# Optimization experiments

Hardware: AMD Instinct MI355X
Metric: run time of the kernel (lower is better)

## Reference

```python
import jax, jax.numpy as jnp
import numpy as np

B, N, E, H = 4, 2048, 1024, 16
D = E // H
SCALE = 1.0 / np.sqrt(D).astype(np.float32)


def setup_inputs() -> dict:
    key = jax.random.key(0)
    ks = jax.random.split(key, 8)
    xq = jax.random.normal(ks[0], (B, N, E), jnp.float32)
    xk = jax.random.normal(ks[1], (B, N, E), jnp.float32)
    xv = jax.random.normal(ks[2], (B, N, E), jnp.float32)
    # causal mask: True means 'masked out' (matches masked_fill_ semantics)
    attn_mask = jnp.triu(jnp.ones((N, N), dtype=bool), k=1)[None, None]
    Wq = jax.random.normal(ks[3], (E, E), jnp.float32) / np.sqrt(E)
    Wk = jax.random.normal(ks[4], (E, E), jnp.float32) / np.sqrt(E)
    Wv = jax.random.normal(ks[5], (E, E), jnp.float32) / np.sqrt(E)
    Wo = jax.random.normal(ks[6], (E, E), jnp.float32) / np.sqrt(E)
    bo = jnp.zeros((E,), jnp.float32)
    return {"xq": xq, "xk": xk, "xv": xv, "attn_mask": attn_mask,
            "Wq": Wq, "Wk": Wk, "Wv": Wv, "Wo": Wo, "bo": bo}


def _split_heads(x):
    # [B, N, E] -> [B, H, N, D]
    return x.reshape(B, N, H, D).transpose(0, 2, 1, 3)


def reference(xq, xk, xv, attn_mask, Wq, Wk, Wv, Wo, bo):
    # torch nn.Linear: y = x @ W.T
    q = _split_heads(xq @ Wq.T)
    k = _split_heads(xk @ Wk.T)
    v = _split_heads(xv @ Wv.T)
    scores = SCALE * jnp.einsum('bhqd,bhkd->bhqk', q, k)
    scores = jnp.where(attn_mask, -jnp.inf, scores)
    attn = jax.nn.softmax(scores, axis=-1)
    out = jnp.einsum('bhqk,bhkd->bhqd', attn, v)
    out = out.transpose(0, 2, 1, 3).reshape(B, N, E)  # merge heads
    return out @ Wo.T + bo
```

## Files before the change

### kernel.cpp

```cpp
#include <hip/hip_runtime.h>
#include <hip/hip_bf16.h>
#include <stdint.h>
#include <stddef.h>

#define B_ 4
#define N_ 2048
#define E_ 1024
#define H_ 16
#define D_ 64

using bf16 = __hip_bfloat16;
typedef __bf16 bf16x8 __attribute__((ext_vector_type(8)));
typedef float  f32x4  __attribute__((ext_vector_type(4)));

__device__ inline bf16x8 load8(const float* p) {
    f32x4 a = *(const f32x4*)p;
    f32x4 b = *(const f32x4*)(p + 4);
    bf16x8 r;
#pragma unroll
    for (int e = 0; e < 4; e++) { r[e] = (__bf16)a[e]; r[e + 4] = (__bf16)b[e]; }
    return r;
}
__device__ inline void store_elem(float* C, size_t idx, float v) { C[idx] = v; }
__device__ inline void store_elem(bf16* C, size_t idx, float v) {
    C[idx] = __float2bfloat16(v);
}

__device__ inline void async_stage16(const bf16* g, bf16* l) {
    __builtin_amdgcn_global_load_lds(
        (const __attribute__((address_space(1))) uint32_t*)g,
        (__attribute__((address_space(3))) uint32_t*)l, 16, 0, 0);
}
__device__ inline void manual_stage16(const float* g, bf16* l) {
    *(bf16x8*)l = load8(g);
}

__global__ __launch_bounds__(256) void cvt_all(
    const float* __restrict__ w0, const float* __restrict__ w1,
    const float* __restrict__ w2, const float* __restrict__ w3,
    bf16* __restrict__ wd,
    const float* __restrict__ x0, const float* __restrict__ x1,
    const float* __restrict__ x2,
    bf16* __restrict__ xd0, bf16* __restrict__ xd1, bf16* __restrict__ xd2)
{
    int bx = blockIdx.x;
    const float* s; bf16* d;
    if (bx < 2048) {
        const int seg = bx >> 9;
        s = seg == 0 ? w0 : seg == 1 ? w1 : seg == 2 ? w2 : w3;
        d = wd + (size_t)seg * (E_ * E_);
        bx &= 511;
    } else {
        bx -= 2048;
        const int seg = bx >> 12;
        s = seg == 0 ? x0 : seg == 1 ? x1 : x2;
        d = seg == 0 ? xd0 : seg == 1 ? xd1 : xd2;
        bx &= 4095;
    }
    const size_t off = ((size_t)bx * 256 + threadIdx.x) * 8;
    *(bf16x8*)&d[off] = load8(s + off);
}

struct GemmB { const void* A[3]; void* C[3]; };

template <typename TA, typename TC>
__global__ __launch_bounds__(256) void gemm_bt(
    GemmB batch, const bf16* __restrict__ Wb, const float* __restrict__ bias)
{
    __shared__ bf16 As[128 * 32];
    __shared__ bf16 Bs[128 * 32];

    const TA*   __restrict__ A = (const TA*)batch.A[blockIdx.z];
    TC*         __restrict__ C = (TC*)batch.C[blockIdx.z];
    const bf16* __restrict__ W = Wb + (size_t)blockIdx.z * (E_ * E_);

    const int tid  = threadIdx.x;
    const int lane = tid & 63;
    const int wave = tid >> 6;
    const int wr   = wave >> 1;
    const int wc   = wave & 1;
    const int r    = lane & 15;
    const int quad = lane >> 4;

    const int m0 = blockIdx.y * 128;
    const int n0 = blockIdx.x * 128;

    const int row0 = tid >> 2,         cc0 = (tid & 3) * 8;
    const int row1 = (tid + 256) >> 2, cc1 = cc0;

    f32x4 acc[4][4];
#pragma unroll
    for (int i = 0; i < 4; i++)
#pragma unroll
        for (int j = 0; j < 4; j++)
            acc[i][j] = {0.0f, 0.0f, 0.0f, 0.0f};

    for (int k0 = 0; k0 < E_; k0 += 32) {
        __syncthreads();
        if constexpr (__is_same(TA, bf16)) {
            async_stage16(&A[(size_t)(m0 + row0) * E_ + k0 + cc0], &As[tid * 8]);
            async_stage16(&A[(size_t)(m0 + row1) * E_ + k0 + cc1], &As[(tid + 256) * 8]);
        } else {
            manual_stage16(&A[(size_t)(m0 + row0) * E_ + k0 + cc0], &As[tid * 8]);
            manual_stage16(&A[(size_t)(m0 + row1) * E_ + k0 + cc1], &As[(tid + 256) * 8]);
        }
        async_stage16(&W[(size_t)(n0 + row0) * E_ + k0 + cc0], &Bs[tid * 8]);
        async_stage16(&W[(size_t)(n0 + row1) * E_ + k0 + cc1], &Bs[(tid + 256) * 8]);
        __syncthreads();

        bf16x8 a[4], b[4];
#pragma unroll
        for (int mt = 0; mt < 4; mt++)
            a[mt] = *(const bf16x8*)&As[(wr * 64 + mt * 16 + r) * 32 + quad * 8];
#pragma unroll
        for (int nt = 0; nt < 4; nt++)
            b[nt] = *(const bf16x8*)&Bs[(wc * 64 + nt * 16 + r) * 32 + quad * 8];
#pragma unroll
        for (int mt = 0; mt < 4; mt++)
#pragma unroll
            for (int nt = 0; nt < 4; nt++)
                acc[mt][nt] = __builtin_amdgcn_mfma_f32_16x16x32_bf16(
                    a[mt], b[nt], acc[mt][nt], 0, 0, 0);
    }

#pragma unroll
    for (int mt = 0; mt < 4; mt++) {
#pragma unroll
        for (int nt = 0; nt < 4; nt++) {
            const int col = n0 + wc * 64 + nt * 16 + r;
            float bv = bias ? bias[col] : 0.0f;
#pragma unroll
            for (int rg = 0; rg < 4; rg++) {
                const int row = m0 + wr * 64 + mt * 16 + quad * 4 + rg;
                store_elem(C, (size_t)row * E_ + col, acc[mt][nt][rg] + bv);
            }
        }
    }
}

__global__ __launch_bounds__(256) void attn_fwd(
    const bf16* __restrict__ q, const bf16* __restrict__ k,
    const bf16* __restrict__ v, bf16* __restrict__ o)
{
    constexpr int LS = 72;
    __shared__ bf16 Ks[64 * LS];
    __shared__ bf16 Vt[64 * LS];
    __shared__ bf16 Ps[128 * LS];

    const int tid  = threadIdx.x;
    const int lane = tid & 63;
    const int wave = tid >> 6;
    const int r    = lane & 15;
    const int quad = lane >> 4;

    const int bh = blockIdx.y;
    const int b  = bh >> 4;
    const int h  = bh & 15;
    const int xb = gridDim.x - 1 - blockIdx.x;
    const int q0 = xb * 128;

    const size_t basek = (size_t)b * N_ * E_ + (size_t)h * D_;

    bf16x8 qB[2][2];
#pragma unroll
    for (int s = 0; s < 2; s++) {
        const size_t qrow =
            ((size_t)b * N_ + q0 + wave * 32 + s * 16 + r) * E_ + h * D_;
        qB[s][0] = *(const bf16x8*)&q[qrow + quad * 8];
        qB[s][1] = *(const bf16x8*)&q[qrow + quad * 8 + 32];
    }

    float m_i[2] = {-1e30f, -1e30f};
    float l_i[2] = {0.0f, 0.0f};
    f32x4 o_acc[4][2];
#pragma unroll
    for (int dt = 0; dt < 4; dt++)
#pragma unroll
        for (int s = 0; s < 2; s++)
            o_acc[dt][s] = {0.0f, 0.0f, 0.0f, 0.0f};

    const int ntiles = 2 * xb + 2;

    const int key0 = tid >> 3;
    const int key1 = key0 + 32;
    const int ck   = (tid & 7) * 8;
    const int kp   = tid & 31;
    const int cv   = (tid >> 5) * 8;

    bf16x8 kpre0 = *(const bf16x8*)&k[basek + (size_t)key0 * E_ + ck];
    bf16x8 kpre1 = *(const bf16x8*)&k[basek + (size_t)key1 * E_ + ck];
    bf16x8 vp0   = *(const bf16x8*)&v[basek + (size_t)(2 * kp) * E_ + cv];
    bf16x8 vp1   = *(const bf16x8*)&v[basek + (size_t)(2 * kp + 1) * E_ + cv];

    for (int t = 0; t < ntiles; t++) {
        __syncthreads();
        *(bf16x8*)&Ks[key0 * LS + ck] = kpre0;
        *(bf16x8*)&Ks[key1 * LS + ck] = kpre1;
#pragma unroll
        for (int e = 0; e < 8; e++) {
            union { __bf16 hh[2]; uint32_t u; } pk;
            pk.hh[0] = vp0[e]; pk.hh[1] = vp1[e];
            *(uint32_t*)&Vt[(cv + e) * LS + 2 * kp] = pk.u;
        }
        __syncthreads();

        if (t + 1 < ntiles) {
            const size_t j1 = (size_t)(t + 1) * 64;
            kpre0 = *(const bf16x8*)&k[basek + (j1 + key0) * E_ + ck];
            kpre1 = *(const bf16x8*)&k[basek + (j1 + key1) * E_ + ck];
            vp0   = *(const bf16x8*)&v[basek + (j1 + 2 * kp) * E_ + cv];
            vp1   = *(const bf16x8*)&v[basek + (j1 + 2 * kp + 1) * E_ + cv];
        }

        f32x4 sf[4][2];
#pragma unroll
        for (int mt = 0; mt < 4; mt++)
#pragma unroll
            for (int s = 0; s < 2; s++)
                sf[mt][s] = {0.0f, 0.0f, 0.0f, 0.0f};
#pragma unroll
        for (int ks = 0; ks < 2; ks++)
#pragma unroll
            for (int mt = 0; mt < 4; mt++) {
                bf16x8 ka = *(const bf16x8*)&Ks[(mt * 16 + r) * LS + ks * 32 + quad * 8];
#pragma unroll
                for (int s = 0; s < 2; s++)
                    sf[mt][s] = __builtin_amdgcn_mfma_f32_16x16x32_bf16(
                        ka, qB[s][ks], sf[mt][s], 0, 0, 0);
            }

        if (t >= ntiles - 2) {
#pragma unroll
            for (int mt = 0; mt < 4; mt++)
#pragma unroll
                for (int s = 0; s < 2; s++) {
                    const int qgl = q0 + wave * 32 + s * 16 + r;
#pragma unroll
                    for (int rg = 0; rg < 4; rg++) {
                        const int kgl = t * 64 + mt * 16 + quad * 4 + rg;
                        sf[mt][s][rg] =
                            (kgl <= qgl) ? sf[mt][s][rg] * 0.125f : -1e30f;
                    }
                }
        } else {
#pragma unroll
            for (int mt = 0; mt < 4; mt++)
#pragma unroll
                for (int s = 0; s < 2; s++)
#pragma unroll
                    for (int rg = 0; rg < 4; rg++)
                        sf[mt][s][rg] *= 0.125f;
        }

#pragma unroll
        for (int s = 0; s < 2; s++) {
            float mx = sf[0][s][0];
#pragma unroll
            for (int mt = 0; mt < 4; mt++)
#pragma unroll
                for (int rg = 0; rg < 4; rg++)
                    mx = fmaxf(mx, sf[mt][s][rg]);
            mx = fmaxf(mx, __shfl_xor(mx, 16));
            mx = fmaxf(mx, __shfl_xor(mx, 32));
            const float m_new = fmaxf(m_i[s], mx);
            const float al = __expf(m_i[s] - m_new);
            m_i[s] = m_new;

            float ls = 0.0f;
            const int prow = (wave * 32 + s * 16 + r) * LS;
#pragma unroll
            for (int mt = 0; mt < 4; mt++) {
                const float p0 = __expf(sf[mt][s][0] - m_new);
                const float p1 = __expf(sf[mt][s][1] - m_new);
                const float p2 = __expf(sf[mt][s][2] - m_new);
                const float p3 = __expf(sf[mt][s][3] - m_new);
                ls += (p0 + p1) + (p2 + p3);
                union { __bf16 hh[4]; uint2 u2; } pk;
                pk.hh[0] = (__bf16)p0; pk.hh[1] = (__bf16)p1;
                pk.hh[2] = (__bf16)p2; pk.hh[3] = (__bf16)p3;
                *(uint2*)&Ps[prow + mt * 16 + quad * 4] = pk.u2;
            }
            ls += __shfl_xor(ls, 16);
            ls += __shfl_xor(ls, 32);
            l_i[s] = l_i[s] * al + ls;
#pragma unroll
            for (int dt = 0; dt < 4; dt++)
#pragma unroll
                for (int rg = 0; rg < 4; rg++)
                    o_acc[dt][s][rg] *= al;
        }

#pragma unroll
        for (int ks = 0; ks < 2; ks++) {
            bf16x8 pb[2];
#pragma unroll
            for (int s = 0; s < 2; s++)
                pb[s] = *(const bf16x8*)
                    &Ps[(wave * 32 + s * 16 + r) * LS + ks * 32 + quad * 8];
#pragma unroll
            for (int dt = 0; dt < 4; dt++) {
                bf16x8 va = *(const bf16x8*)&Vt[(dt * 16 + r) * LS + ks * 32 + quad * 8];
#pragma unroll
                for (int s = 0; s < 2; s++)
                    o_acc[dt][s] = __builtin_amdgcn_mfma_f32_16x16x32_bf16(
                        va, pb[s], o_acc[dt][s], 0, 0, 0);
            }
        }
    }

#pragma unroll
    for (int s = 0; s < 2; s++) {
        const float invl = 1.0f / l_i[s];
        const size_t orow =
            ((size_t)b * N_ + q0 + wave * 32 + s * 16 + r) * E_ + h * D_;
#pragma unroll
        for (int dt = 0; dt < 4; dt++) {
            union { __bf16 hh[4]; uint2 u2; } pk;
#pragma unroll
            for (int rg = 0; rg < 4; rg++)
                pk.hh[rg] = (__bf16)(o_acc[dt][s][rg] * invl);
            *(uint2*)&o[orow + dt * 16 + quad * 4] = pk.u2;
        }
    }
}

extern "C" void kernel_launch(void* const* d_in, const int* in_sizes, int n_in,
                              void* d_out, int out_size, void* d_ws, size_t ws_size,
                              hipStream_t stream) {
    const float* xq = (const float*)d_in[0];
    const float* xk = (const float*)d_in[1];
    const float* xv = (const float*)d_in[2];
    const float* Wq = (const float*)d_in[4];
    const float* Wk = (const float*)d_in[5];
    const float* Wv = (const float*)d_in[6];
    const float* Wo = (const float*)d_in[7];
    const float* bo = (const float*)d_in[8];
    float* out = (float*)d_out;

    const size_t elems = (size_t)B_ * N_ * E_;
    const size_t wel   = (size_t)E_ * E_;
    bf16* q   = (bf16*)d_ws;
    bf16* kk  = q + elems;
    bf16* vv  = kk + elems;
    bf16* ao  = vv + elems;
    bf16* Wb  = ao + elems;
    bf16* xb0 = Wb + 4 * wel;
    bf16* xb1 = xb0 + elems;
    bf16* xb2 = xb1 + elems;

    const size_t need_big = (7 * elems + 4 * wel) * 2;
    const bool big = ws_size >= need_big;

    dim3 blk(256);
    if (big) {
        cvt_all<<<dim3(14336), blk, 0, stream>>>(
            Wq, Wk, Wv, Wo, Wb, xq, xk, xv, xb0, xb1, xb2);
    } else {
        cvt_all<<<dim3(2048), blk, 0, stream>>>(
            Wq, Wk, Wv, Wo, Wb, nullptr, nullptr, nullptr,
            nullptr, nullptr, nullptr);
    }

    GemmB proj;
    if (big) { proj.A[0] = xb0; proj.A[1] = xb1; proj.A[2] = xb2; }
    else     { proj.A[0] = xq;  proj.A[1] = xk;  proj.A[2] = xv;  }
    proj.C[0] = q; proj.C[1] = kk; proj.C[2] = vv;
    if (big)
        gemm_bt<bf16, bf16><<<dim3(E_ / 128, (B_ * N_) / 128, 3), blk, 0, stream>>>(
            proj, Wb, nullptr);
    else
        gemm_bt<float, bf16><<<dim3(E_ / 128, (B_ * N_) / 128, 3), blk, 0, stream>>>(
            proj, Wb, nullptr);

    attn_fwd<<<dim3(N_ / 128, B_ * H_), blk, 0, stream>>>(q, kk, vv, ao);

    GemmB fin;
    fin.A[0] = ao; fin.A[1] = ao; fin.A[2] = ao;
    fin.C[0] = out; fin.C[1] = out; fin.C[2] = out;
    gemm_bt<bf16, float><<<dim3(E_ / 128, (B_ * N_) / 128, 1), blk, 0, stream>>>(
        fin, Wb + 3 * wel, bo);
}
```

Measured before the change: 396.4 us.

## Pair causal query blocks per workgroup and double-buffer K/V tiles in attention

Each attention workgroup now processes two query blocks (p and 15-p), so every block handles the same number of causal key tiles. This balances load across a grid half the previous size. K/V shared tiles are double-buffered with a two-ahead register prefetch, which drops one barrier per tile. The softmax scale is folded into Q before the bf16 MFMA, adding a second bf16 rounding of Q and doubling K/V LDS use, which may reduce occupancy.

```diff
diff --git a/kernel.cpp b/kernel.cpp
--- a/kernel.cpp
+++ b/kernel.cpp
@@ -143,8 +143,8 @@
     const bf16* __restrict__ v, bf16* __restrict__ o)
 {
     constexpr int LS = 72;
-    __shared__ bf16 Ks[64 * LS];
-    __shared__ bf16 Vt[64 * LS];
+    __shared__ bf16 Ks[2][64 * LS];
+    __shared__ bf16 Vt[2][64 * LS];
     __shared__ bf16 Ps[128 * LS];
 
     const int tid  = threadIdx.x;
@@ -156,30 +156,9 @@
     const int bh = blockIdx.y;
     const int b  = bh >> 4;
     const int h  = bh & 15;
-    const int xb = gridDim.x - 1 - blockIdx.x;
-    const int q0 = xb * 128;
+    const int p  = blockIdx.x;
 
     const size_t basek = (size_t)b * N_ * E_ + (size_t)h * D_;
-
-    bf16x8 qB[2][2];
-#pragma unroll
-    for (int s = 0; s < 2; s++) {
-        const size_t qrow =
-            ((size_t)b * N_ + q0 + wave * 32 + s * 16 + r) * E_ + h * D_;
-        qB[s][0] = *(const bf16x8*)&q[qrow + quad * 8];
-        qB[s][1] = *(const bf16x8*)&q[qrow + quad * 8 + 32];
-    }
-
-    float m_i[2] = {-1e30f, -1e30f};
-    float l_i[2] = {0.0f, 0.0f};
-    f32x4 o_acc[4][2];
-#pragma unroll
-    for (int dt = 0; dt < 4; dt++)
-#pragma unroll
-        for (int s = 0; s < 2; s++)
-            o_acc[dt][s] = {0.0f, 0.0f, 0.0f, 0.0f};
-
-    const int ntiles = 2 * xb + 2;
 
     const int key0 = tid >> 3;
     const int key1 = key0 + 32;
@@ -187,139 +166,182 @@
     const int kp   = tid & 31;
     const int cv   = (tid >> 5) * 8;
 
-    bf16x8 kpre0 = *(const bf16x8*)&k[basek + (size_t)key0 * E_ + ck];
-    bf16x8 kpre1 = *(const bf16x8*)&k[basek + (size_t)key1 * E_ + ck];
-    bf16x8 vp0   = *(const bf16x8*)&v[basek + (size_t)(2 * kp) * E_ + cv];
-    bf16x8 vp1   = *(const bf16x8*)&v[basek + (size_t)(2 * kp + 1) * E_ + cv];
-
-    for (int t = 0; t < ntiles; t++) {
-        __syncthreads();
-        *(bf16x8*)&Ks[key0 * LS + ck] = kpre0;
-        *(bf16x8*)&Ks[key1 * LS + ck] = kpre1;
+#pragma unroll
+    for (int ph = 0; ph < 2; ph++) {
+        const int xb = ph == 0 ? (15 - p) : p;
+        const int q0 = xb * 128;
+        const int nt = 2 * xb + 2;
+
+        bf16x8 qB[2][2];
+#pragma unroll
+        for (int s = 0; s < 2; s++) {
+            const size_t qrow =
+                ((size_t)b * N_ + q0 + wave * 32 + s * 16 + r) * E_ + h * D_;
+            qB[s][0] = *(const bf16x8*)&q[qrow + quad * 8];
+            qB[s][1] = *(const bf16x8*)&q[qrow + quad * 8 + 32];
+#pragma unroll
+            for (int ks = 0; ks < 2; ks++)
+#pragma unroll
+                for (int e = 0; e < 8; e++)
+                    qB[s][ks][e] = (__bf16)((float)qB[s][ks][e] * 0.125f);
+        }
+
+        float m_i[2] = {-1e30f, -1e30f};
+        float l_i[2] = {0.0f, 0.0f};
+        f32x4 o_acc[4][2];
+#pragma unroll
+        for (int dt = 0; dt < 4; dt++)
+#pragma unroll
+            for (int s = 0; s < 2; s++)
+                o_acc[dt][s] = {0.0f, 0.0f, 0.0f, 0.0f};
+
+        bf16x8 kp0, kp1, vp0, vp1;
+        kp0 = *(const bf16x8*)&k[basek + (size_t)key0 * E_ + ck];
+        kp1 = *(const bf16x8*)&k[basek + (size_t)key1 * E_ + ck];
+        vp0 = *(const bf16x8*)&v[basek + (size_t)(2 * kp) * E_ + cv];
+        vp1 = *(const bf16x8*)&v[basek + (size_t)(2 * kp + 1) * E_ + cv];
+        *(bf16x8*)&Ks[0][key0 * LS + ck] = kp0;
+        *(bf16x8*)&Ks[0][key1 * LS + ck] = kp1;
 #pragma unroll
         for (int e = 0; e < 8; e++) {
             union { __bf16 hh[2]; uint32_t u; } pk;
             pk.hh[0] = vp0[e]; pk.hh[1] = vp1[e];
-            *(uint32_t*)&Vt[(cv + e) * LS + 2 * kp] = pk.u;
+            *(uint32_t*)&Vt[0][(cv + e) * LS + 2 * kp] = pk.u;
+        }
+        {
+            const size_t j1 = 64;
+            kp0 = *(const bf16x8*)&k[basek + (j1 + key0) * E_ + ck];
+            kp1 = *(const bf16x8*)&k[basek + (j1 + key1) * E_ + ck];
+            vp0 = *(const bf16x8*)&v[basek + (j1 + 2 * kp) * E_ + cv];
+            vp1 = *(const bf16x8*)&v[basek + (j1 + 2 * kp + 1) * E_ + cv];
         }
         __syncthreads();
 
-        if (t + 1 < ntiles) {
-            const size_t j1 = (size_t)(t + 1) * 64;
-            kpre0 = *(const bf16x8*)&k[basek + (j1 + key0) * E_ + ck];
-            kpre1 = *(const bf16x8*)&k[basek + (j1 + key1) * E_ + ck];
-            vp0   = *(const bf16x8*)&v[basek + (j1 + 2 * kp) * E_ + cv];
-            vp1   = *(const bf16x8*)&v[basek + (j1 + 2 * kp + 1) * E_ + cv];
-        }
-
-        f32x4 sf[4][2];
-#pragma unroll
-        for (int mt = 0; mt < 4; mt++)
-#pragma unroll
-            for (int s = 0; s < 2; s++)
-                sf[mt][s] = {0.0f, 0.0f, 0.0f, 0.0f};
-#pragma unroll
-        for (int ks = 0; ks < 2; ks++)
-#pragma unroll
-            for (int mt = 0; mt < 4; mt++) {
-                bf16x8 ka = *(const bf16x8*)&Ks[(mt * 16 + r) * LS + ks * 32 + quad * 8];
+        for (int t = 0; t < nt; t++) {
+            const int cur = t & 1;
+
+            if (t + 1 < nt) {
+                *(bf16x8*)&Ks[cur ^ 1][key0 * LS + ck] = kp0;
+                *(bf16x8*)&Ks[cur ^ 1][key1 * LS + ck] = kp1;
+#pragma unroll
+                for (int e = 0; e < 8; e++) {
+                    union { __bf16 hh[2]; uint32_t u; } pk;
+                    pk.hh[0] = vp0[e]; pk.hh[1] = vp1[e];
+                    *(uint32_t*)&Vt[cur ^ 1][(cv + e) * LS + 2 * kp] = pk.u;
+                }
+            }
+            if (t + 2 < nt) {
+                const size_t j2 = (size_t)(t + 2) * 64;
+                kp0 = *(const bf16x8*)&k[basek + (j2 + key0) * E_ + ck];
+                kp1 = *(const bf16x8*)&k[basek + (j2 + key1) * E_ + ck];
+                vp0 = *(const bf16x8*)&v[basek + (j2 + 2 * kp) * E_ + cv];
+                vp1 = *(const bf16x8*)&v[basek + (j2 + 2 * kp + 1) * E_ + cv];
+            }
+
+            f32x4 sf[4][2];
+#pragma unroll
+            for (int mt = 0; mt < 4; mt++)
 #pragma unroll
                 for (int s = 0; s < 2; s++)
-                    sf[mt][s] = __builtin_amdgcn_mfma_f32_16x16x32_bf16(
-                        ka, qB[s][ks], sf[mt][s], 0, 0, 0);
-            }
-
-        if (t >= ntiles - 2) {
-#pragma unroll
-            for (int mt = 0; mt < 4; mt++)
-#pragma unroll
-                for (int s = 0; s < 2; s++) {
-                    const int qgl = q0 + wave * 32 + s * 16 + r;
-#pragma unroll
-                    for (int rg = 0; rg < 4; rg++) {
-                        const int kgl = t * 64 + mt * 16 + quad * 4 + rg;
-                        sf[mt][s][rg] =
-                            (kgl <= qgl) ? sf[mt][s][rg] * 0.125f : -1e30f;
+                    sf[mt][s] = {0.0f, 0.0f, 0.0f, 0.0f};
+#pragma unroll
+            for (int ks = 0; ks < 2; ks++)
+#pragma unroll
+                for (int mt = 0; mt < 4; mt++) {
+                    bf16x8 ka = *(const bf16x8*)
+                        &Ks[cur][(mt * 16 + r) * LS + ks * 32 + quad * 8];
+#pragma unroll
+                    for (int s = 0; s < 2; s++)
+                        sf[mt][s] = __builtin_amdgcn_mfma_f32_16x16x32_bf16(
+                            ka, qB[s][ks], sf[mt][s], 0, 0, 0);
+                }
+
+            if (t >= nt - 2) {
+#pragma unroll
+                for (int mt = 0; mt < 4; mt++)
+#pragma unroll
+                    for (int s = 0; s < 2; s++) {
+                        const int qgl = q0 + wave * 32 + s * 16 + r;
+#pragma unroll
+                        for (int rg = 0; rg < 4; rg++) {
+                            const int kgl = t * 64 + mt * 16 + quad * 4 + rg;
+                            if (kgl > qgl) sf[mt][s][rg] = -1e30f;
+                        }
                     }
+            }
+
+#pragma unroll
+            for (int s = 0; s < 2; s++) {
+                float mx = sf[0][s][0];
+#pragma unroll
+                for (int mt = 0; mt < 4; mt++)
+#pragma unroll
+                    for (int rg = 0; rg < 4; rg++)
+                        mx = fmaxf(mx, sf[mt][s][rg]);
+                mx = fmaxf(mx, __shfl_xor(mx, 16));
+                mx = fmaxf(mx, __shfl_xor(mx, 32));
+                const float m_new = fmaxf(m_i[s], mx);
+                const float al = __expf(m_i[s] - m_new);
+                m_i[s] = m_new;
+
+                float ls = 0.0f;
+                const int prow = (wave * 32 + s * 16 + r) * LS;
+#pragma unroll
+                for (int mt = 0; mt < 4; mt++) {
+                    const float p0 = __expf(sf[mt][s][0] - m_new);
+                    const float p1 = __expf(sf[mt][s][1] - m_new);
+                    const float p2 = __expf(sf[mt][s][2] - m_new);
+                    const float p3 = __expf(sf[mt][s][3] - m_new);
+                    ls += (p0 + p1) + (p2 + p3);
+                    union { __bf16 hh[4]; uint2 u2; } pk;
+                    pk.hh[0] = (__bf16)p0; pk.hh[1] = (__bf16)p1;
+                    pk.hh[2] = (__bf16)p2; pk.hh[3] = (__bf16)p3;
+                    *(uint2*)&Ps[prow + mt * 16 + quad * 4] = pk.u2;
                 }
-        } else {
-#pragma unroll
-            for (int mt = 0; mt < 4; mt++)
+                ls += __shfl_xor(ls, 16);
+                ls += __shfl_xor(ls, 32);
+                l_i[s] = l_i[s] * al + ls;
+#pragma unroll
+                for (int dt = 0; dt < 4; dt++)
+#pragma unroll
+                    for (int rg = 0; rg < 4; rg++)
+                        o_acc[dt][s][rg] *= al;
+            }
+
+#pragma unroll
+            for (int ks = 0; ks < 2; ks++) {
+                bf16x8 pb[2];
 #pragma unroll
                 for (int s = 0; s < 2; s++)
-#pragma unroll
-                    for (int rg = 0; rg < 4; rg++)
-                        sf[mt][s][rg] *= 0.125f;
+                    pb[s] = *(const bf16x8*)
+                        &Ps[(wave * 32 + s * 16 + r) * LS + ks * 32 + quad * 8];
+#pragma unroll
+                for (int dt = 0; dt < 4; dt++) {
+                    bf16x8 va = *(const bf16x8*)
+                        &Vt[cur][(dt * 16 + r) * LS + ks * 32 + quad * 8];
+#pragma unroll
+                    for (int s = 0; s < 2; s++)
+                        o_acc[dt][s] = __builtin_amdgcn_mfma_f32_16x16x32_bf16(
+                            va, pb[s], o_acc[dt][s], 0, 0, 0);
+                }
+            }
+
+            __syncthreads();
         }
 
 #pragma unroll
         for (int s = 0; s < 2; s++) {
-            float mx = sf[0][s][0];
-#pragma unroll
-            for (int mt = 0; mt < 4; mt++)
+            const float invl = 1.0f / l_i[s];
+            const size_t orow =
+                ((size_t)b * N_ + q0 + wave * 32 + s * 16 + r) * E_ + h * D_;
+#pragma unroll
+            for (int dt = 0; dt < 4; dt++) {
+                union { __bf16 hh[4]; uint2 u2; } pk;
 #pragma unroll
                 for (int rg = 0; rg < 4; rg++)
-                    mx = fmaxf(mx, sf[mt][s][rg]);
-            mx = fmaxf(mx, __shfl_xor(mx, 16));
-            mx = fmaxf(mx, __shfl_xor(mx, 32));
-            const float m_new = fmaxf(m_i[s], mx);
-            const float al = __expf(m_i[s] - m_new);
-            m_i[s] = m_new;
-
-            float ls = 0.0f;
-            const int prow = (wave * 32 + s * 16 + r) * LS;
-#pragma unroll
-            for (int mt = 0; mt < 4; mt++) {
-                const float p0 = __expf(sf[mt][s][0] - m_new);
-                const float p1 = __expf(sf[mt][s][1] - m_new);
-                const float p2 = __expf(sf[mt][s][2] - m_new);
-                const float p3 = __expf(sf[mt][s][3] - m_new);
-                ls += (p0 + p1) + (p2 + p3);
-                union { __bf16 hh[4]; uint2 u2; } pk;
-                pk.hh[0] = (__bf16)p0; pk.hh[1] = (__bf16)p1;
-                pk.hh[2] = (__bf16)p2; pk.hh[3] = (__bf16)p3;
-                *(uint2*)&Ps[prow + mt * 16 + quad * 4] = pk.u2;
-            }
-            ls += __shfl_xor(ls, 16);
-            ls += __shfl_xor(ls, 32);
-            l_i[s] = l_i[s] * al + ls;
-#pragma unroll
-            for (int dt = 0; dt < 4; dt++)
-#pragma unroll
-                for (int rg = 0; rg < 4; rg++)
-                    o_acc[dt][s][rg] *= al;
-        }
-
-#pragma unroll
-        for (int ks = 0; ks < 2; ks++) {
-            bf16x8 pb[2];
-#pragma unroll
-            for (int s = 0; s < 2; s++)
-                pb[s] = *(const bf16x8*)
-                    &Ps[(wave * 32 + s * 16 + r) * LS + ks * 32 + quad * 8];
-#pragma unroll
-            for (int dt = 0; dt < 4; dt++) {
-                bf16x8 va = *(const bf16x8*)&Vt[(dt * 16 + r) * LS + ks * 32 + quad * 8];
-#pragma unroll
-                for (int s = 0; s < 2; s++)
-                    o_acc[dt][s] = __builtin_amdgcn_mfma_f32_16x16x32_bf16(
-                        va, pb[s], o_acc[dt][s], 0, 0, 0);
-            }
-        }
-    }
-
-#pragma unroll
-    for (int s = 0; s < 2; s++) {
-        const float invl = 1.0f / l_i[s];
-        const size_t orow =
-            ((size_t)b * N_ + q0 + wave * 32 + s * 16 + r) * E_ + h * D_;
-#pragma unroll
-        for (int dt = 0; dt < 4; dt++) {
-            union { __bf16 hh[4]; uint2 u2; } pk;
-#pragma unroll
-            for (int rg = 0; rg < 4; rg++)
-                pk.hh[rg] = (__bf16)(o_acc[dt][s][rg] * invl);
-            *(uint2*)&o[orow + dt * 16 + quad * 4] = pk.u2;
+                    pk.hh[rg] = (__bf16)(o_acc[dt][s][rg] * invl);
+                *(uint2*)&o[orow + dt * 16 + quad * 4] = pk.u2;
+            }
         }
     }
 }
@@ -372,7 +394,7 @@
         gemm_bt<float, bf16><<<dim3(E_ / 128, (B_ * N_) / 128, 3), blk, 0, stream>>>(
             proj, Wb, nullptr);
 
-    attn_fwd<<<dim3(N_ / 128, B_ * H_), blk, 0, stream>>>(q, kk, vv, ao);
+    attn_fwd<<<dim3(8, B_ * H_), blk, 0, stream>>>(q, kk, vv, ao);
 
     GemmB fin;
     fin.A[0] = ao; fin.A[1] = ao; fin.A[2] = ao;
```

Result: faster. 345.8 us (-12.8%).
